# Kernel optimization log

Measured on AMD Instinct MI355X. Metric: run time of the kernel, lower is better.

## Reference

```python
import jax, jax.numpy as jnp
import numpy as np
import math

B, S, D, NH, L = 4, 1024, 512, 8, 2
PRED, COUT = 96, 512
DH = D // NH
EPS_BACKEND = 1e-6
EPS_LN = 1e-5


def setup_inputs() -> dict:
    key = jax.random.key(0)
    ks = jax.random.split(key, 8)
    return {
        "x_enc": jax.random.normal(ks[0], (B, S, D), jnp.float32),
        "x_mark_enc": jax.random.normal(ks[1], (B, S, 4), jnp.float32),
        "x_dec": jax.random.normal(ks[2], (B, PRED, D), jnp.float32),
        "x_mark_dec": jax.random.normal(ks[3], (B, PRED, 4), jnp.float32),
        # per-layer mLSTM cell params (stacked over L layers)
        "W_ig": jax.random.normal(ks[4], (L, NH, 3 * D), jnp.float32) * 0.02,
        "b_ig": jnp.zeros((L, NH), jnp.float32),
        "W_fg": jax.random.normal(ks[5], (L, NH, 3 * D), jnp.float32) * 0.02,
        "b_fg": jnp.zeros((L, NH), jnp.float32),
        "ln_w": jnp.ones((L, D), jnp.float32),
        # final head
        "fc_W": jax.random.normal(ks[6], (COUT, D), jnp.float32) * 0.02,
        "fc_b": jnp.zeros((COUT,), jnp.float32),
    }


def _mlstm_cell(q, k, v, W_ig, b_ig, W_fg, b_fg, ln_w):
    """xlstm parallel_stabilized_simple backend + MultiHeadLayerNorm."""
    Bq, Sq, Dq = q.shape
    gate_in = jnp.concatenate([q, k, v], axis=-1)          # [B,S,3D]
    ig = jnp.einsum('bsd,hd->bhs', gate_in, W_ig) + b_ig[None, :, None]  # [B,NH,S]
    fg = jnp.einsum('bsd,hd->bhs', gate_in, W_fg) + b_fg[None, :, None]  # [B,NH,S]

    qh = q.reshape(Bq, Sq, NH, DH).transpose(0, 2, 1, 3)   # [B,NH,S,DH]
    kh = k.reshape(Bq, Sq, NH, DH).transpose(0, 2, 1, 3)
    vh = v.reshape(Bq, Sq, NH, DH).transpose(0, 2, 1, 3)

    log_f = jax.nn.log_sigmoid(fg)                          # [B,NH,S]
    fcum = jnp.cumsum(log_f, axis=-1)                       # F[i] = sum_{t<=i} log_f[t]
    # log_fg_matrix[i,j] = F[i] - F[j] for j<=i, else -inf
    lfg = fcum[..., :, None] - fcum[..., None, :]           # [B,NH,S,S]
    causal = jnp.tril(jnp.ones((Sq, Sq), dtype=bool))
    log_D = jnp.where(causal, lfg + ig[..., None, :], -jnp.inf)  # [B,NH,S,S]

    max_log_D = jnp.max(log_D, axis=-1, keepdims=True)      # row-wise stabilizer
    Dm = jnp.exp(log_D - max_log_D)

    qk = jnp.einsum('bhsd,bhtd->bhst', qh, kh) * (1.0 / math.sqrt(DH))
    C = qk * Dm
    normalizer = jnp.maximum(jnp.abs(jnp.sum(C, axis=-1, keepdims=True)),
                             jnp.exp(-max_log_D))
    Cn = C / (normalizer + EPS_BACKEND)
    h = jnp.einsum('bhst,bhtd->bhsd', Cn, vh)               # [B,NH,S,DH]

    # MultiHeadLayerNorm == GroupNorm over DH per head, weight only (no bias)
    mu = jnp.mean(h, axis=-1, keepdims=True)
    var = jnp.var(h, axis=-1, keepdims=True)
    hn = (h - mu) * jax.lax.rsqrt(var + EPS_LN)
    hn = hn * ln_w.reshape(NH, DH)[None, :, None, :]
    return hn.transpose(0, 2, 1, 3).reshape(Bq, Sq, Dq)     # [B,S,D]


def reference(x_enc, x_mark_enc, x_dec, x_mark_dec,
              W_ig, b_ig, W_fg, b_fg, ln_w, fc_W, fc_b):
    q = x_enc
    k = x_enc
    v = x_enc
    for l in range(L):
        q = _mlstm_cell(q, k, v, W_ig[l], b_ig[l], W_fg[l], b_fg[l], ln_w[l])
    dec_out = jnp.einsum('bsd,od->bso', q[:, -PRED:, :], fc_W) + fc_b
    return dec_out
```

## Files before the change

kernel.cpp:

```cpp
#include <hip/hip_runtime.h>
#include <hip/hip_bf16.h>
#include <math.h>
#include <stdint.h>

#define B_ 4
#define S_ 1024
#define D_ 512
#define NH_ 8
#define DH_ 64
#define L_ 2
#define PRED_ 96
#define COUT_ 512

typedef __attribute__((ext_vector_type(8))) short short8;
typedef __attribute__((ext_vector_type(4))) float f32x4;

__device__ __forceinline__ unsigned short f2bf(float f) {
  union { float f; unsigned int u; } v; v.f = f;
  unsigned int r = v.u + 0x7fffu + ((v.u >> 16) & 1u);
  return (unsigned short)(r >> 16);
}
__device__ __forceinline__ float bf2f(unsigned short h) {
  union { unsigned int u; float f; } v; v.u = (unsigned int)h << 16;
  return v.f;
}

__global__ __launch_bounds__(64) void convkv_kernel(
    const float* __restrict__ x, unsigned short* __restrict__ hiA,
    unsigned short* __restrict__ loA) {
  int bs = blockIdx.x;
  int b = bs >> 10, s = bs & 1023;
  int t = threadIdx.x;
  int h = t >> 3, dh0 = (t & 7) * 8;
  const float* src = x + (size_t)bs * D_ + t * 8;
  float4 v0 = *(const float4*)(src);
  float4 v1 = *(const float4*)(src + 4);
  float xv[8] = {v0.x, v0.y, v0.z, v0.w, v1.x, v1.y, v1.z, v1.w};
  unsigned short hh[8], ll[8];
#pragma unroll
  for (int k = 0; k < 8; ++k) {
    hh[k] = f2bf(xv[k]);
    ll[k] = f2bf(xv[k] - bf2f(hh[k]));
  }
  size_t off = (((size_t)(b * NH_ + h)) * S_ + s) * 64 + dh0;
  *(uint4*)(hiA + off) = *(const uint4*)hh;
  *(uint4*)(loA + off) = *(const uint4*)ll;
}

__global__ __launch_bounds__(256) void transpose_kernel(
    const unsigned short* __restrict__ src_a, unsigned short* __restrict__ dst_a) {
  int jt = blockIdx.x, h = blockIdx.y, b = blockIdx.z;
  int bh = b * NH_ + h, j0 = jt * 64;
  __shared__ unsigned short tile[64][72];
  int t = threadIdx.x;
  {
    int j = t >> 2, dseg = (t & 3) * 16;
    const unsigned short* src = src_a + ((size_t)bh * S_ + j0 + j) * 64 + dseg;
    uint4 a0 = *(const uint4*)(src);
    uint4 a1 = *(const uint4*)(src + 8);
    *(uint4*)(&tile[j][dseg]) = a0;
    *(uint4*)(&tile[j][dseg + 8]) = a1;
  }
  __syncthreads();
  {
    int d = t >> 2, jseg = (t & 3) * 16;
    unsigned short us[16];
#pragma unroll
    for (int k = 0; k < 16; ++k) us[k] = tile[jseg + k][d];
    unsigned short* dst = dst_a + ((size_t)bh * 64 + d) * S_ + j0 + jseg;
    *(uint4*)(dst) = *(const uint4*)us;
    *(uint4*)(dst + 8) = *(const uint4*)(us + 8);
  }
}

__global__ __launch_bounds__(256) void gates2_kernel(
    const float* __restrict__ q, const float* __restrict__ x,
    const float* __restrict__ Wig, const float* __restrict__ big,
    const float* __restrict__ Wfg, const float* __restrict__ bfg,
    float* __restrict__ ig_out, float* __restrict__ fg_out) {
  int sc = blockIdx.x, hg = blockIdx.y, b = blockIdx.z;
  __shared__ float Wq_s[8][512];
  __shared__ float Wc_s[8][512];
  for (int idx = threadIdx.x; idx < 8 * 512; idx += 256) {
    int p = idx >> 9, e = idx & 511;
    int h = hg * 4 + (p >> 1);
    const float* Wr = ((p & 1) ? Wfg : Wig) + (size_t)h * (3 * D_);
    Wq_s[p][e] = Wr[e];
    Wc_s[p][e] = Wr[512 + e] + Wr[1024 + e];
  }
  __syncthreads();
  int wv = threadIdx.x >> 6, l = threadIdx.x & 63;
  for (int rr = 0; rr < 8; ++rr) {
    int s = sc * 32 + wv * 8 + rr;
    const float* qrow = q + ((size_t)(b * S_ + s)) * D_;
    const float* xrow = x + ((size_t)(b * S_ + s)) * D_;
    float ql[8], xl[8];
#pragma unroll
    for (int k = 0; k < 8; ++k) { ql[k] = qrow[l + 64 * k]; xl[k] = xrow[l + 64 * k]; }
#pragma unroll
    for (int p = 0; p < 8; ++p) {
      float acc = 0.f;
#pragma unroll
      for (int k = 0; k < 8; ++k)
        acc += Wq_s[p][l + 64 * k] * ql[k] + Wc_s[p][l + 64 * k] * xl[k];
#pragma unroll
      for (int off = 32; off; off >>= 1) acc += __shfl_down(acc, off);
      if (l == 0) {
        int h = hg * 4 + (p >> 1);
        float v = acc + ((p & 1) ? bfg : big)[h];
        ((p & 1) ? fg_out : ig_out)[((size_t)(b * NH_ + h)) * S_ + s] = v;
      }
    }
  }
}

__global__ __launch_bounds__(64) void scan_kernel(
    const float* __restrict__ ig, const float* __restrict__ fg,
    float* __restrict__ a_out, float* __restrict__ amax_out) {
  int bh = blockIdx.x;
  int lane = threadIdx.x;
  const float* igr = ig + (size_t)bh * S_;
  const float* fgr = fg + (size_t)bh * S_;
  const int CH = S_ / 64;
  float lf[16], av[16];
  float lsum = 0.f;
  int base = lane * CH;
  for (int u = 0; u < CH; ++u) {
    float xv = fgr[base + u];
    float ls = (xv >= 0.f) ? -log1pf(__expf(-xv)) : (xv - log1pf(__expf(xv)));
    lf[u] = ls; lsum += ls;
  }
  float pref = lsum;
#pragma unroll
  for (int off = 1; off < 64; off <<= 1) {
    float t = __shfl_up(pref, off);
    if (lane >= off) pref += t;
  }
  float F = pref - lsum;
  float lamax = -INFINITY;
  for (int u = 0; u < CH; ++u) {
    F += lf[u];
    float a = igr[base + u] - F;
    av[u] = a;
    lamax = fmaxf(lamax, a);
  }
  float pmax = lamax;
#pragma unroll
  for (int off = 1; off < 64; off <<= 1) {
    float t = __shfl_up(pmax, off);
    if (lane >= off) pmax = fmaxf(pmax, t);
  }
  float run = __shfl_up(pmax, 1);
  if (lane == 0) run = -INFINITY;
  for (int u = 0; u < CH; ++u) {
    run = fmaxf(run, av[u]);
    size_t o = (size_t)bh * S_ + base + u;
    a_out[o] = av[u];
    amax_out[o] = run;
  }
}

__global__ __launch_bounds__(256) void attn_mfma_kernel(
    const float* __restrict__ qin,
    const unsigned short* __restrict__ kH, const unsigned short* __restrict__ kL,
    const unsigned short* __restrict__ tH, const unsigned short* __restrict__ tL,
    const float* __restrict__ a_arr, const float* __restrict__ amax_arr,
    const float* __restrict__ lnw, float* __restrict__ out,
    int it0, int orow0, int out_srows) {
  int it = blockIdx.x + it0, h = blockIdx.y, b = blockIdx.z;
  int i0 = it * 64;
  int bh = b * NH_ + h;
  int tid = threadIdx.x;
  int w = tid >> 6, l = tid & 63;
  int l15 = l & 15, lg = l >> 4;

  __shared__ __align__(16) unsigned char smem[49152 + 256];
  unsigned char* KsH = smem;
  unsigned char* KsL = smem + 8192;
  unsigned char* VtH = smem + 16384;
  unsigned char* VtL = smem + 24576;
  unsigned char* PwH = smem + 32768 + w * 2048;
  unsigned char* PwL = smem + 40960 + w * 2048;
  float* aLds = (float*)(smem + 49152);

  short8 qh[2], qlo[2];
  {
    const float* qrow = qin + ((size_t)(b * S_ + i0 + w * 16 + l15)) * D_ + h * DH_;
#pragma unroll
    for (int ks = 0; ks < 2; ++ks) {
      const float* p = qrow + ks * 32 + lg * 8;
      float4 v0 = *(const float4*)(p);
      float4 v1 = *(const float4*)(p + 4);
      float xv[8] = {v0.x, v0.y, v0.z, v0.w, v1.x, v1.y, v1.z, v1.w};
      unsigned short hh[8], ll[8];
#pragma unroll
      for (int k = 0; k < 8; ++k) {
        hh[k] = f2bf(xv[k]);
        ll[k] = f2bf(xv[k] - bf2f(hh[k]));
      }
      qh[ks] = *(const short8*)hh;
      qlo[ks] = *(const short8*)ll;
    }
  }
  float am_i = amax_arr[(size_t)bh * S_ + i0 + w * 16 + l15];
  const float* abase = a_arr + (size_t)bh * S_;

  f32x4 acc[4];
#pragma unroll
  for (int nt = 0; nt < 4; ++nt) acc[nt] = (f32x4){0.f, 0.f, 0.f, 0.f};

  const unsigned short* KsrcH = kH + (size_t)bh * S_ * 64;
  const unsigned short* KsrcL = kL + (size_t)bh * S_ * 64;
  const unsigned short* TsrcH = tH + (size_t)bh * 64 * S_;
  const unsigned short* TsrcL = tL + (size_t)bh * 64 * S_;

  for (int jt = 0; jt <= it; ++jt) {
    int j0 = jt * 64;
    __syncthreads();
    {
      int r = w * 16 + l15;
#pragma unroll
      for (int gb = 0; gb < 8; gb += 4) {
        int g = gb + lg;
        int sw = r * 128 + ((g ^ (r & 7)) * 16);
        *(uint4*)(KsH + sw) = *(const uint4*)(KsrcH + ((size_t)(j0 + r)) * 64 + g * 8);
        *(uint4*)(KsL + sw) = *(const uint4*)(KsrcL + ((size_t)(j0 + r)) * 64 + g * 8);
        *(uint4*)(VtH + sw) = *(const uint4*)(TsrcH + (size_t)r * S_ + j0 + g * 8);
        *(uint4*)(VtL + sw) = *(const uint4*)(TsrcL + (size_t)r * S_ + j0 + g * 8);
      }
    }
    if (tid < 64) aLds[tid] = abase[j0 + tid];
    __syncthreads();
    int i_g = i0 + w * 16 + l15;
#pragma unroll
    for (int js = 0; js < 4; ++js) {
      f32x4 st = (f32x4){0.f, 0.f, 0.f, 0.f};
      int krow = js * 16 + l15;
      int key = krow & 7;
      short8 kh0 = *(const short8*)(KsH + krow * 128 + (((0 + lg) ^ key) * 16));
      short8 kh1 = *(const short8*)(KsH + krow * 128 + (((4 + lg) ^ key) * 16));
      short8 kl0 = *(const short8*)(KsL + krow * 128 + (((0 + lg) ^ key) * 16));
      short8 kl1 = *(const short8*)(KsL + krow * 128 + (((4 + lg) ^ key) * 16));
      st = __builtin_amdgcn_mfma_f32_16x16x32_bf16(kh0, qh[0], st, 0, 0, 0);
      st = __builtin_amdgcn_mfma_f32_16x16x32_bf16(kh1, qh[1], st, 0, 0, 0);
      st = __builtin_amdgcn_mfma_f32_16x16x32_bf16(kh0, qlo[0], st, 0, 0, 0);
      st = __builtin_amdgcn_mfma_f32_16x16x32_bf16(kh1, qlo[1], st, 0, 0, 0);
      st = __builtin_amdgcn_mfma_f32_16x16x32_bf16(kl0, qh[0], st, 0, 0, 0);
      st = __builtin_amdgcn_mfma_f32_16x16x32_bf16(kl1, qh[1], st, 0, 0, 0);
      int jb_loc = js * 16 + lg * 4;
      unsigned int pkh[2], pkl[2];
#pragma unroll
      for (int r2 = 0; r2 < 2; ++r2) {
        unsigned int ph = 0, pl = 0;
#pragma unroll
        for (int rr = 0; rr < 2; ++rr) {
          int r = r2 * 2 + rr;
          int jl = jb_loc + r;
          float e = __expf(fminf(aLds[jl] - am_i, 0.f));
          float wv = (j0 + jl <= i_g) ? st[r] * 0.125f * e : 0.f;
          unsigned short whi = f2bf(wv);
          unsigned short wlo = f2bf(wv - bf2f(whi));
          ph |= (unsigned int)whi << (rr * 16);
          pl |= (unsigned int)wlo << (rr * 16);
        }
        pkh[r2] = ph; pkl[r2] = pl;
      }
      int g = js * 2 + (lg >> 1);
      int pw_off = l15 * 128 + ((g ^ (l15 & 7)) * 16) + (lg & 1) * 8;
      *(uint2*)(PwH + pw_off) = make_uint2(pkh[0], pkh[1]);
      *(uint2*)(PwL + pw_off) = make_uint2(pkl[0], pkl[1]);
    }
#pragma unroll
    for (int ks = 0; ks < 2; ++ks) {
      int pg = ((ks * 4 + lg) ^ (l15 & 7)) * 16;
      short8 ph = *(const short8*)(PwH + l15 * 128 + pg);
      short8 pl = *(const short8*)(PwL + l15 * 128 + pg);
#pragma unroll
      for (int nt = 0; nt < 4; ++nt) {
        int vr = nt * 16 + l15;
        int vg = vr * 128 + (((ks * 4 + lg) ^ (vr & 7)) * 16);
        short8 vh = *(const short8*)(VtH + vg);
        short8 vl = *(const short8*)(VtL + vg);
        acc[nt] = __builtin_amdgcn_mfma_f32_16x16x32_bf16(ph, vh, acc[nt], 0, 0, 0);
        acc[nt] = __builtin_amdgcn_mfma_f32_16x16x32_bf16(pl, vh, acc[nt], 0, 0, 0);
        acc[nt] = __builtin_amdgcn_mfma_f32_16x16x32_bf16(ph, vl, acc[nt], 0, 0, 0);
      }
    }
  }

  float lw[4];
#pragma unroll
  for (int nt = 0; nt < 4; ++nt) lw[nt] = lnw[h * DH_ + nt * 16 + l15];
#pragma unroll
  for (int r = 0; r < 4; ++r) {
    int il = lg * 4 + r;
    int i_glob = i0 + w * 16 + il;
    float hv[4], s1 = 0.f, s2 = 0.f;
#pragma unroll
    for (int nt = 0; nt < 4; ++nt) {
      hv[nt] = acc[nt][r];
      s1 += hv[nt]; s2 += hv[nt] * hv[nt];
    }
#pragma unroll
    for (int off = 1; off < 16; off <<= 1) {
      s1 += __shfl_xor(s1, off); s2 += __shfl_xor(s2, off);
    }
    float mean = s1 * (1.f / 64.f);
    float var = s2 * (1.f / 64.f) - mean * mean;
    float rstd = rsqrtf(var + 1e-5f);
    float* orow = out + ((size_t)(b * out_srows + (i_glob - orow0))) * D_ + h * DH_;
#pragma unroll
    for (int nt = 0; nt < 4; ++nt)
      orow[nt * 16 + l15] = (hv[nt] - mean) * rstd * lw[nt];
  }
}

__global__ __launch_bounds__(256) void fc2_kernel(
    const float* __restrict__ q2c, const float* __restrict__ W,
    const float* __restrict__ bias, float* __restrict__ out) {
  int blk = blockIdx.x;
  __shared__ float qs[3][512];
  for (int idx = threadIdx.x; idx < 3 * 512; idx += 256) {
    int rr = idx >> 9, e = idx & 511;
    int bp = blk * 3 + rr;
    int b = bp / PRED_, pcol = bp % PRED_;
    qs[rr][e] = q2c[((size_t)(b * 128 + 32 + pcol)) * D_ + e];
  }
  __syncthreads();
  int wv = threadIdx.x >> 6, l = threadIdx.x & 63;
  for (int o = wv; o < COUT_; o += 4) {
    const float* Wr = W + (size_t)o * D_;
    float a0 = 0.f, a1 = 0.f, a2 = 0.f;
#pragma unroll
    for (int k = 0; k < 8; ++k) {
      float wvv = Wr[l + 64 * k];
      a0 += wvv * qs[0][l + 64 * k];
      a1 += wvv * qs[1][l + 64 * k];
      a2 += wvv * qs[2][l + 64 * k];
    }
#pragma unroll
    for (int off = 32; off; off >>= 1) {
      a0 += __shfl_down(a0, off); a1 += __shfl_down(a1, off); a2 += __shfl_down(a2, off);
    }
    if (l == 0) {
      float bs = bias[o];
      float av[3] = {a0, a1, a2};
      for (int rr = 0; rr < 3; ++rr)
        out[(size_t)(blk * 3 + rr) * COUT_ + o] = av[rr] + bs;
    }
  }
}

extern "C" void kernel_launch(void* const* d_in, const int* in_sizes, int n_in,
                              void* d_out, int out_size, void* d_ws, size_t ws_size,
                              hipStream_t stream) {
  const float* x_enc = (const float*)d_in[0];
  const float* W_ig = (const float*)d_in[4];
  const float* b_ig = (const float*)d_in[5];
  const float* W_fg = (const float*)d_in[6];
  const float* b_fg = (const float*)d_in[7];
  const float* ln_w = (const float*)d_in[8];
  const float* fc_W = (const float*)d_in[9];
  const float* fc_b = (const float*)d_in[10];

  float* ws = (float*)d_ws;
  const size_t NBSD = (size_t)B_ * S_ * D_;
  const size_t NBHS = (size_t)B_ * NH_ * S_;
  float* h1 = ws;
  float* h2c = h1 + NBSD;
  float* ig = h2c + (size_t)B_ * 128 * D_;
  float* fg = ig + NBHS;
  float* aA = fg + NBHS;
  float* amaxA = aA + NBHS;
  unsigned short* kvhH = (unsigned short*)(amaxA + NBHS);
  unsigned short* kvhL = kvhH + NBSD;
  unsigned short* kvTH = kvhL + NBSD;
  unsigned short* kvTL = kvTH + NBSD;

  convkv_kernel<<<B_ * S_, 64, 0, stream>>>(x_enc, kvhH, kvhL);
  transpose_kernel<<<dim3(S_ / 64, NH_, B_), 256, 0, stream>>>(kvhH, kvTH);
  transpose_kernel<<<dim3(S_ / 64, NH_, B_), 256, 0, stream>>>(kvhL, kvTL);

  for (int l = 0; l < L_; ++l) {
    const float* qin = (l == 0) ? x_enc : h1;
    gates2_kernel<<<dim3(S_ / 32, 2, B_), 256, 0, stream>>>(
        qin, x_enc,
        W_ig + (size_t)l * NH_ * 3 * D_, b_ig + (size_t)l * NH_,
        W_fg + (size_t)l * NH_ * 3 * D_, b_fg + (size_t)l * NH_, ig, fg);
    scan_kernel<<<B_ * NH_, 64, 0, stream>>>(ig, fg, aA, amaxA);
    if (l == 0) {
      attn_mfma_kernel<<<dim3(S_ / 64, NH_, B_), 256, 0, stream>>>(
          qin, kvhH, kvhL, kvTH, kvTL, aA, amaxA, ln_w + (size_t)l * D_,
          h1, 0, 0, S_);
    } else {
      attn_mfma_kernel<<<dim3(2, NH_, B_), 256, 0, stream>>>(
          qin, kvhH, kvhL, kvTH, kvTL, aA, amaxA, ln_w + (size_t)l * D_,
          h2c, 14, 896, 128);
    }
  }
  fc2_kernel<<<B_ * PRED_ / 3, 256, 0, stream>>>(h2c, fc_W, fc_b, (float*)d_out);
}
```

Before: 350.8 us.

## Replace scalar FC head with split-bf16 MFMA kernel fed by bf16 attention output

The final projection is now done by an MFMA kernel using a three-term hi/lo bf16 split to approximate fp32 accuracy, instead of a scalar dot-product kernel with shuffle reductions. The layer-2 attention kernel writes its normalized output directly as hi/lo bf16 pairs so the new head can load operands as short8 vectors. The weights are converted to hi/lo bf16 on the fly in every block, which adds conversion ALU work and redundant weight reads across row tiles. The new head launches only 48 blocks.

```diff
diff --git a/kernel.cpp b/kernel.cpp
--- a/kernel.cpp
+++ b/kernel.cpp
@@ -166,7 +166,8 @@
     const unsigned short* __restrict__ tH, const unsigned short* __restrict__ tL,
     const float* __restrict__ a_arr, const float* __restrict__ amax_arr,
     const float* __restrict__ lnw, float* __restrict__ out,
-    int it0, int orow0, int out_srows) {
+    unsigned short* __restrict__ outH, unsigned short* __restrict__ outL,
+    int write_bf, int it0, int orow0, int out_srows) {
   int it = blockIdx.x + it0, h = blockIdx.y, b = blockIdx.z;
   int i0 = it * 64;
   int bh = b * NH_ + h;
@@ -308,46 +309,72 @@
     float mean = s1 * (1.f / 64.f);
     float var = s2 * (1.f / 64.f) - mean * mean;
     float rstd = rsqrtf(var + 1e-5f);
-    float* orow = out + ((size_t)(b * out_srows + (i_glob - orow0))) * D_ + h * DH_;
-#pragma unroll
-    for (int nt = 0; nt < 4; ++nt)
-      orow[nt * 16 + l15] = (hv[nt] - mean) * rstd * lw[nt];
-  }
-}
-
-__global__ __launch_bounds__(256) void fc2_kernel(
-    const float* __restrict__ q2c, const float* __restrict__ W,
-    const float* __restrict__ bias, float* __restrict__ out) {
-  int blk = blockIdx.x;
-  __shared__ float qs[3][512];
-  for (int idx = threadIdx.x; idx < 3 * 512; idx += 256) {
-    int rr = idx >> 9, e = idx & 511;
-    int bp = blk * 3 + rr;
-    int b = bp / PRED_, pcol = bp % PRED_;
-    qs[rr][e] = q2c[((size_t)(b * 128 + 32 + pcol)) * D_ + e];
-  }
-  __syncthreads();
-  int wv = threadIdx.x >> 6, l = threadIdx.x & 63;
-  for (int o = wv; o < COUT_; o += 4) {
-    const float* Wr = W + (size_t)o * D_;
-    float a0 = 0.f, a1 = 0.f, a2 = 0.f;
-#pragma unroll
-    for (int k = 0; k < 8; ++k) {
-      float wvv = Wr[l + 64 * k];
-      a0 += wvv * qs[0][l + 64 * k];
-      a1 += wvv * qs[1][l + 64 * k];
-      a2 += wvv * qs[2][l + 64 * k];
-    }
-#pragma unroll
-    for (int off = 32; off; off >>= 1) {
-      a0 += __shfl_down(a0, off); a1 += __shfl_down(a1, off); a2 += __shfl_down(a2, off);
-    }
-    if (l == 0) {
-      float bs = bias[o];
-      float av[3] = {a0, a1, a2};
-      for (int rr = 0; rr < 3; ++rr)
-        out[(size_t)(blk * 3 + rr) * COUT_ + o] = av[rr] + bs;
-    }
+    size_t ro = ((size_t)(b * out_srows + (i_glob - orow0))) * D_ + h * DH_;
+    if (!write_bf) {
+#pragma unroll
+      for (int nt = 0; nt < 4; ++nt)
+        out[ro + nt * 16 + l15] = (hv[nt] - mean) * rstd * lw[nt];
+    } else {
+#pragma unroll
+      for (int nt = 0; nt < 4; ++nt) {
+        float v = (hv[nt] - mean) * rstd * lw[nt];
+        unsigned short hi = f2bf(v);
+        outH[ro + nt * 16 + l15] = hi;
+        outL[ro + nt * 16 + l15] = f2bf(v - bf2f(hi));
+      }
+    }
+  }
+}
+
+__global__ __launch_bounds__(256) void fc3_kernel(
+    const unsigned short* __restrict__ qH, const unsigned short* __restrict__ qL,
+    const float* __restrict__ W, const float* __restrict__ bias,
+    float* __restrict__ out) {
+  int rt = blockIdx.x, ot = blockIdx.y;
+  int tid = threadIdx.x;
+  int w = tid >> 6, l = tid & 63, l15 = l & 15, lg = l >> 4;
+  int r_flat = rt * 64 + w * 16 + l15;
+  int b = r_flat / 96, pc = r_flat - b * 96;
+  const unsigned short* qHrow = qH + ((size_t)(b * 128 + 32 + pc)) * D_;
+  const unsigned short* qLrow = qL + ((size_t)(b * 128 + 32 + pc)) * D_;
+  int obase = ot * 64;
+
+  f32x4 acc[4];
+#pragma unroll
+  for (int og = 0; og < 4; ++og) acc[og] = (f32x4){0.f, 0.f, 0.f, 0.f};
+
+#pragma unroll 2
+  for (int ks = 0; ks < 16; ++ks) {
+    int k0 = ks * 32 + lg * 8;
+    short8 ah = *(const short8*)(qHrow + k0);
+    short8 al = *(const short8*)(qLrow + k0);
+#pragma unroll
+    for (int og = 0; og < 4; ++og) {
+      const float* wrow = W + (size_t)(obase + og * 16 + l15) * D_ + k0;
+      float4 w0 = *(const float4*)(wrow);
+      float4 w1 = *(const float4*)(wrow + 4);
+      float wv[8] = {w0.x, w0.y, w0.z, w0.w, w1.x, w1.y, w1.z, w1.w};
+      unsigned short bhh[8], bll[8];
+#pragma unroll
+      for (int k = 0; k < 8; ++k) {
+        bhh[k] = f2bf(wv[k]);
+        bll[k] = f2bf(wv[k] - bf2f(bhh[k]));
+      }
+      short8 bh = *(const short8*)bhh;
+      short8 bl = *(const short8*)bll;
+      acc[og] = __builtin_amdgcn_mfma_f32_16x16x32_bf16(ah, bh, acc[og], 0, 0, 0);
+      acc[og] = __builtin_amdgcn_mfma_f32_16x16x32_bf16(al, bh, acc[og], 0, 0, 0);
+      acc[og] = __builtin_amdgcn_mfma_f32_16x16x32_bf16(ah, bl, acc[og], 0, 0, 0);
+    }
+  }
+  int rbase = rt * 64 + w * 16 + lg * 4;
+#pragma unroll
+  for (int og = 0; og < 4; ++og) {
+    int o = obase + og * 16 + l15;
+    float bs = bias[o];
+#pragma unroll
+    for (int r = 0; r < 4; ++r)
+      out[(size_t)(rbase + r) * COUT_ + o] = acc[og][r] + bs;
   }
 }
 
@@ -367,8 +394,7 @@
   const size_t NBSD = (size_t)B_ * S_ * D_;
   const size_t NBHS = (size_t)B_ * NH_ * S_;
   float* h1 = ws;
-  float* h2c = h1 + NBSD;
-  float* ig = h2c + (size_t)B_ * 128 * D_;
+  float* ig = h1 + NBSD;
   float* fg = ig + NBHS;
   float* aA = fg + NBHS;
   float* amaxA = aA + NBHS;
@@ -376,6 +402,8 @@
   unsigned short* kvhL = kvhH + NBSD;
   unsigned short* kvTH = kvhL + NBSD;
   unsigned short* kvTL = kvTH + NBSD;
+  unsigned short* hqH = kvTL + NBSD;
+  unsigned short* hqL = hqH + (size_t)B_ * 128 * D_;
 
   convkv_kernel<<<B_ * S_, 64, 0, stream>>>(x_enc, kvhH, kvhL);
   transpose_kernel<<<dim3(S_ / 64, NH_, B_), 256, 0, stream>>>(kvhH, kvTH);
@@ -391,12 +419,12 @@
     if (l == 0) {
       attn_mfma_kernel<<<dim3(S_ / 64, NH_, B_), 256, 0, stream>>>(
           qin, kvhH, kvhL, kvTH, kvTL, aA, amaxA, ln_w + (size_t)l * D_,
-          h1, 0, 0, S_);
+          h1, (unsigned short*)nullptr, (unsigned short*)nullptr, 0, 0, 0, S_);
     } else {
       attn_mfma_kernel<<<dim3(2, NH_, B_), 256, 0, stream>>>(
           qin, kvhH, kvhL, kvTH, kvTL, aA, amaxA, ln_w + (size_t)l * D_,
-          h2c, 14, 896, 128);
-    }
-  }
-  fc2_kernel<<<B_ * PRED_ / 3, 256, 0, stream>>>(h2c, fc_W, fc_b, (float*)d_out);
-}
+          (float*)nullptr, hqH, hqL, 1, 14, 896, 128);
+    }
+  }
+  fc3_kernel<<<dim3(6, 8), 256, 0, stream>>>(hqH, hqL, fc_W, fc_b, (float*)d_out);
+}
```

Measured after the change: 299.0 us. 1.17x faster.
